# Kernel optimization log

Hardware: AMD Instinct MI355X
Metric: run time of the kernel (lower is better)

The kernel has to match this reference:

```python
import jax, jax.numpy as jnp
import numpy as np
import math

INPUT_DIM = 1024
QUERY_DIM = 1024
VALUE_DIM = 1024

def setup_inputs() -> dict:
    key = jax.random.key(0)
    ks = jax.random.split(key, 7)
    N, T, D = 4, 4096, INPUT_DIM
    s_in = 1.0 / math.sqrt(D)
    X = jax.random.normal(ks[0], (N, T, D), dtype=jnp.float32)
    # torch.nn.Linear weights: (out, in), init ~ U(-1/sqrt(in), 1/sqrt(in))
    Wq = jax.random.uniform(ks[1], (QUERY_DIM, D), jnp.float32, -s_in, s_in)
    bq = jax.random.uniform(ks[2], (QUERY_DIM,), jnp.float32, -s_in, s_in)
    Wk = jax.random.uniform(ks[3], (QUERY_DIM, D), jnp.float32, -s_in, s_in)
    bk = jax.random.uniform(ks[4], (QUERY_DIM,), jnp.float32, -s_in, s_in)
    Wv = jax.random.uniform(ks[5], (VALUE_DIM, D), jnp.float32, -s_in, s_in)
    bv = jax.random.uniform(ks[6], (VALUE_DIM,), jnp.float32, -s_in, s_in)
    return {"X": X, "Wq": Wq, "bq": bq, "Wk": Wk, "bk": bk, "Wv": Wv, "bv": bv}

def reference(X, Wq, bq, Wk, bk, Wv, bv):
    N, T, D = X.shape
    q = jnp.einsum('ntd,qd->ntq', X, Wq) + bq  # (N,T,Q)
    k = jnp.einsum('ntd,qd->ntq', X, Wk) + bk  # (N,T,Q)
    v = jnp.einsum('ntd,vd->ntv', X, Wv) + bv  # (N,T,V)
    # NOTE: original scales by sqrt(D) = sqrt(input_dim), not sqrt(query_dim)
    scores = jnp.einsum('ntq,nsq->nts', q, k) / jnp.sqrt(jnp.asarray(D, X.dtype))
    attn = jax.nn.softmax(scores, axis=-1)  # (N,T,T)
    return jnp.einsum('nts,nsv->ntv', attn, v)
```

## Files before the change

### kernel.cpp

```cpp
#include <hip/hip_runtime.h>
#include <stdint.h>

typedef unsigned short u16;
typedef unsigned char u8;
typedef unsigned int u32;
typedef short shortx8 __attribute__((ext_vector_type(8)));
typedef float floatx4 __attribute__((ext_vector_type(4)));
typedef int intx4 __attribute__((ext_vector_type(4)));
typedef int intx8 __attribute__((ext_vector_type(8)));

__device__ __forceinline__ u16 f2bf(float f) {
    u32 u = __builtin_bit_cast(u32, f);
    u = (u + 0x7fffu + ((u >> 16) & 1u)) >> 16;
    return (u16)u;
}

#if defined(__has_builtin)
#  if __has_builtin(__builtin_amdgcn_cvt_pk_fp8_f32)
#    define HAVE_CVT_FP8 1
#  endif
#  if __has_builtin(__builtin_amdgcn_global_load_lds)
#    define HAVE_GLL 1
#  endif
#endif
#ifndef HAVE_CVT_FP8
#  define HAVE_CVT_FP8 0
#endif
#ifndef HAVE_GLL
#  define HAVE_GLL 0
#endif

__device__ __forceinline__ u8 f2fp8(float f) {
#if HAVE_CVT_FP8
    return (u8)(__builtin_amdgcn_cvt_pk_fp8_f32(f, f, 0, false) & 0xff);
#else
    u32 u = __builtin_bit_cast(u32, f);
    u32 s = (u >> 24) & 0x80u;
    u32 m = u & 0x7fffffffu;
    if (m >= 0x43e00000u) return (u8)(s | 0x7eu);
    if (m < 0x3c800000u) {
        int q = __float2int_rn(__builtin_bit_cast(float, m) * 512.f);
        return (u8)(s | (u32)q);
    }
    u32 r = m + 0x7ffffu + ((m >> 20) & 1u);
    u32 code = (((r >> 23) - 120u) << 3) | ((r >> 20) & 7u);
    if (code > 0x7eu) code = 0x7eu;
    return (u8)(s | code);
#endif
}

#if HAVE_GLL
__device__ __forceinline__ void gload_lds16(const void* g, void* l) {
    __builtin_amdgcn_global_load_lds(
        (const __attribute__((address_space(1))) u32*)g,
        (__attribute__((address_space(3))) u32*)l,
        16, 0, 0);
}
#endif

template <typename OutT, int MODE, int SWZ>
__global__ __launch_bounds__(256, 2) void gemm_bt(
    const u16* __restrict__ Ag, const u16* __restrict__ Bg, OutT* __restrict__ Cg,
    int lda, int ldb, int ldc, int K,
    const float* __restrict__ aux, float scale,
    long long sAz, long long sBz, long long sCz, long long sXz,
    int swz_nhalf)
{
    __shared__ u16 smem[4][128 * 32];

    int z, mb, nb;
    if constexpr (SWZ) {
        const int f = blockIdx.x, xcd = f & 7, g = f >> 3;
        z = xcd >> 1;
        mb = g & 31;
        nb = (xcd & 1) * swz_nhalf + (g >> 5);
    } else {
        z = blockIdx.z; mb = blockIdx.y; nb = blockIdx.x;
    }
    const int m0 = mb * 128, n0 = nb * 128;

    const u16* A = Ag + (long long)z * sAz;
    const u16* B = Bg + (long long)z * sBz;
    OutT* C = Cg + (long long)z * sCz;
    const float* auxp = aux ? aux + (long long)z * sXz : nullptr;

    const int tid = threadIdx.x, lane = tid & 63, wv = tid >> 6;

    const int srow = lane >> 2;
    const int schunk = (lane & 3) * 8;
    const u16* gA0 = A + (size_t)(m0 + wv * 16 + srow) * lda + schunk;
    const u16* gA1 = gA0 + (size_t)64 * lda;
    const u16* gB0 = B + (size_t)(n0 + wv * 16 + srow) * ldb + schunk;
    const u16* gB1 = gB0 + (size_t)64 * ldb;
    const int wb = wv * 512;

    const int wm = (wv & 1) * 64, wn = (wv >> 1) * 64;
    const int mi = lane & 15, kq = lane >> 4;

    floatx4 acc[4][4] = {};

    for (int k0 = 0; k0 < K; k0 += 64) {
#if HAVE_GLL
        gload_lds16(gA0,      &smem[0][wb]);
        gload_lds16(gA1,      &smem[0][2048 + wb]);
        gload_lds16(gA0 + 32, &smem[1][wb]);
        gload_lds16(gA1 + 32, &smem[1][2048 + wb]);
        gload_lds16(gB0,      &smem[2][wb]);
        gload_lds16(gB1,      &smem[2][2048 + wb]);
        gload_lds16(gB0 + 32, &smem[3][wb]);
        gload_lds16(gB1 + 32, &smem[3][2048 + wb]);
#else
        *(shortx8*)(&smem[0][wb] + lane * 8)        = *(const shortx8*)gA0;
        *(shortx8*)(&smem[0][2048 + wb] + lane * 8) = *(const shortx8*)gA1;
        *(shortx8*)(&smem[1][wb] + lane * 8)        = *(const shortx8*)(gA0 + 32);
        *(shortx8*)(&smem[1][2048 + wb] + lane * 8) = *(const shortx8*)(gA1 + 32);
        *(shortx8*)(&smem[2][wb] + lane * 8)        = *(const shortx8*)gB0;
        *(shortx8*)(&smem[2][2048 + wb] + lane * 8) = *(const shortx8*)gB1;
        *(shortx8*)(&smem[3][wb] + lane * 8)        = *(const shortx8*)(gB0 + 32);
        *(shortx8*)(&smem[3][2048 + wb] + lane * 8) = *(const shortx8*)(gB1 + 32);
#endif
        gA0 += 64; gA1 += 64; gB0 += 64; gB1 += 64;
        __syncthreads();

#pragma unroll
        for (int h = 0; h < 2; h++) {
            const u16* Ap = smem[h];
            const u16* Bp = smem[2 + h];
            shortx8 af[4], bfr[4];
#pragma unroll
            for (int i = 0; i < 4; i++)
                af[i] = *(const shortx8*)(Ap + (wm + i * 16 + mi) * 32 + kq * 8);
#pragma unroll
            for (int j = 0; j < 4; j++)
                bfr[j] = *(const shortx8*)(Bp + (wn + j * 16 + mi) * 32 + kq * 8);
#pragma unroll
            for (int i = 0; i < 4; i++)
#pragma unroll
                for (int j = 0; j < 4; j++)
                    acc[i][j] = __builtin_amdgcn_mfma_f32_16x16x32_bf16(
                        af[i], bfr[j], acc[i][j], 0, 0, 0);
        }
        __syncthreads();
    }

    float cb[4];
    if constexpr (MODE == 1) {
#pragma unroll
        for (int j = 0; j < 4; j++) cb[j] = auxp[n0 + wn + j * 16 + mi];
    }

    if constexpr (sizeof(OutT) == 2) {
        u16* ct = &smem[0][0];
#pragma unroll
        for (int i = 0; i < 4; i++) {
#pragma unroll
            for (int r = 0; r < 4; r++) {
                const int lrow = wm + i * 16 + kq * 4 + r;
                float radd = 0.f;
                if constexpr (MODE == 2) radd = auxp[m0 + lrow];
#pragma unroll
                for (int j = 0; j < 4; j++) {
                    float v = acc[i][j][r];
                    if constexpr (MODE == 1) v += cb[j];
                    if constexpr (MODE == 2) v += radd;
                    ct[lrow * 128 + wn + j * 16 + mi] = f2bf(v);
                }
            }
        }
        __syncthreads();
#pragma unroll
        for (int it = 0; it < 8; it++) {
            const int fl = (it * 256 + tid) * 8;
            const int row = fl >> 7, col = fl & 127;
            *(uint4*)(C + (size_t)(m0 + row) * ldc + n0 + col) =
                *(const uint4*)(ct + fl);
        }
    } else if constexpr (sizeof(OutT) == 1) {
        u8* ct = (u8*)&smem[0][0];
#pragma unroll
        for (int i = 0; i < 4; i++) {
#pragma unroll
            for (int r = 0; r < 4; r++) {
                const int lrow = wm + i * 16 + kq * 4 + r;
#pragma unroll
                for (int j = 0; j < 4; j++) {
                    float v = acc[i][j][r];
                    if constexpr (MODE == 1) v += cb[j];
                    ct[lrow * 128 + wn + j * 16 + mi] = f2fp8(v);
                }
            }
        }
        __syncthreads();
        u8* base = (u8*)Cg + ((size_t)mb * 16 + nb) * 16384;
#pragma unroll
        for (int it = 0; it < 4; it++) {
            const int fl = (it * 256 + tid) * 16;
            const int row = fl >> 7, c = (fl >> 4) & 7;
            *(uint4*)(base + row * 128 + ((c ^ (row & 7)) << 4)) =
                *(const uint4*)(ct + fl);
        }
    } else {
#pragma unroll
        for (int i = 0; i < 4; i++) {
#pragma unroll
            for (int r = 0; r < 4; r++) {
                const int row = m0 + wm + i * 16 + kq * 4 + r;
                float rmul = 1.f;
                if constexpr (MODE == 4) rmul = 1.0f / auxp[row];
                OutT* crow = C + (size_t)row * ldc;
#pragma unroll
                for (int j = 0; j < 4; j++) {
                    const int col = n0 + wn + j * 16 + mi;
                    crow[col] = acc[i][j][r] * rmul;
                }
            }
        }
    }
}

__global__ __launch_bounds__(512, 2) void gemm_pv256(
    const u16* __restrict__ Pg, const u16* __restrict__ Vt,
    float* __restrict__ outg, const float* __restrict__ sums, int T, int NT)
{
    __shared__ u8 smem[2][65536];

    const int f = blockIdx.x, xcd = f & 7, g = f >> 3;
    const int z = xcd >> 1;
    const int nb = (xcd & 1) * 2 + (g >> 4);
    const int mb = g & 15;
    const int m0 = mb * 256, n0 = nb * 256;

    const u8* Pz = (const u8*)(Pg + (size_t)z * T * T);
    const u8* Vz = (const u8*)(Vt + (size_t)z * T);
    const float* sumz = sums + (size_t)z * T;

    const int tid = threadIdx.x, lane = tid & 63, wv = tid >> 6;
    const int wr = wv >> 2, wc = wv & 3;
    const int mi = lane & 15, kq = lane >> 4;

    const int srow = lane >> 3;
    const int schunk = ((lane & 7) ^ srow) << 4;
    const size_t ldPb = (size_t)T * 2, ldVb = (size_t)NT * 2;
    const u8* gsrc;
    size_t grstride;
    int lds_r0;
    if (wv < 4) {
        gsrc = Pz + (size_t)(m0 + wv * 64 + srow) * ldPb + schunk;
        grstride = ldPb * 8;
        lds_r0 = wv * 8192;
    } else {
        gsrc = Vz + (size_t)(n0 + (wv - 4) * 64 + srow) * ldVb + schunk;
        grstride = ldVb * 8;
        lds_r0 = 32768 + (wv - 4) * 8192;
    }

    const int csw0 = ((0 * 4 + kq) ^ (mi & 7)) << 4;
    const int csw1 = ((1 * 4 + kq) ^ (mi & 7)) << 4;

    floatx4 acc[8][4] = {};

    auto stage = [&](int slot, int kt) {
        const u8* s0 = gsrc + (size_t)kt * 128;
        u8* l0 = &smem[slot][lds_r0];
#if HAVE_GLL
#pragma unroll
        for (int q = 0; q < 8; q++)
            gload_lds16(s0 + (size_t)q * grstride, l0 + q * 1024);
#else
#pragma unroll
        for (int q = 0; q < 8; q++)
            *(uint4*)(l0 + q * 1024 + lane * 16) =
                *(const uint4*)(s0 + (size_t)q * grstride);
#endif
    };

    stage(0, 0);
    __syncthreads();

    for (int kt = 0; kt < 64; kt++) {
        const int s = kt & 1;
        if (kt < 63) stage(s ^ 1, kt + 1);
        __builtin_amdgcn_sched_barrier(0);

        const u8* Ab = &smem[s][0];
        const u8* Bb = &smem[s][32768];

        shortx8 bfr[4][2];
#pragma unroll
        for (int nj = 0; nj < 4; nj++) {
            const u8* p = Bb + (wc * 64 + nj * 16 + mi) * 128;
            bfr[nj][0] = *(const shortx8*)(p + csw0);
            bfr[nj][1] = *(const shortx8*)(p + csw1);
        }
#pragma unroll
        for (int mh = 0; mh < 2; mh++) {
            shortx8 af[4][2];
#pragma unroll
            for (int fi = 0; fi < 4; fi++) {
                const u8* p = Ab + (wr * 128 + (mh * 4 + fi) * 16 + mi) * 128;
                af[fi][0] = *(const shortx8*)(p + csw0);
                af[fi][1] = *(const shortx8*)(p + csw1);
            }
            __builtin_amdgcn_s_setprio(1);
#pragma unroll
            for (int ks = 0; ks < 2; ks++)
#pragma unroll
                for (int fi = 0; fi < 4; fi++)
#pragma unroll
                    for (int nj = 0; nj < 4; nj++)
                        acc[mh * 4 + fi][nj] = __builtin_amdgcn_mfma_f32_16x16x32_bf16(
                            af[fi][ks], bfr[nj][ks], acc[mh * 4 + fi][nj], 0, 0, 0);
            __builtin_amdgcn_s_setprio(0);
        }
        __syncthreads();
    }

#pragma unroll
    for (int fr = 0; fr < 8; fr++) {
#pragma unroll
        for (int r = 0; r < 4; r++) {
            const int row = m0 + wr * 128 + fr * 16 + kq * 4 + r;
            const float rmul = 1.0f / sumz[row];
            float* crow = outg + ((size_t)z * T + row) * 1024 + n0 + wc * 64 + mi;
#pragma unroll
            for (int nj = 0; nj < 4; nj++)
                crow[nj * 16] = acc[fr][nj][r] * rmul;
        }
    }
}

__device__ __forceinline__ intx8 cat8(intx4 a, intx4 b) {
    return __builtin_shufflevector(a, b, 0, 1, 2, 3, 4, 5, 6, 7);
}

template <int SWZ>
__global__ __launch_bounds__(256, 1) void gemm_fp8_scores(
    const u8* __restrict__ QKt, u16* __restrict__ Pg,
    float* __restrict__ sums, float scale, int T)
{
    __shared__ u8 smem[4][16384];

    int z, mb, nb;
    if constexpr (SWZ) {
        const int f = blockIdx.x, xcd = f & 7, g = f >> 3;
        z = xcd >> 1;
        const int s = g >> 7, t = g & 127;
        mb = (s << 3) | (t & 7);
        nb = (xcd & 1) * 16 + (t >> 3);
    } else {
        z = blockIdx.z; mb = blockIdx.y; nb = blockIdx.x;
    }
    const int m0 = mb * 128, n0 = nb * 128;

    const u8* At = QKt + ((size_t)(z * 32 + mb) * 16) * 16384;
    const u8* Bt = QKt + ((size_t)(z * 32 + nb) * 16 + 8) * 16384;
    u16* P = Pg + (size_t)z * T * T;
    float* sumz = sums + (size_t)z * T;

    const int tid = threadIdx.x, lane = tid & 63, wv = tid >> 6;
    const int wm = (wv & 1) * 64, wn = (wv >> 1) * 64;
    const int mi = lane & 15, kq = lane >> 4;
    const int xm = mi & 7;
    const int off0 = ((2 * kq) ^ xm) * 16;
    const int off1 = ((2 * kq + 1) ^ xm) * 16;

    const u8* gA = At + wv * 4096 + lane * 16;
    const u8* gB = Bt + wv * 4096 + lane * 16;

    floatx4 acc[4][4] = {};

#if HAVE_GLL
#pragma unroll
    for (int i = 0; i < 4; i++) {
        gload_lds16(gA + i * 1024, &smem[0][wv * 4096] + i * 1024);
        gload_lds16(gB + i * 1024, &smem[1][wv * 4096] + i * 1024);
    }
#else
#pragma unroll
    for (int i = 0; i < 4; i++) {
        *(uint4*)(&smem[0][wv * 4096] + i * 1024 + lane * 16) = *(const uint4*)(gA + i * 1024);
        *(uint4*)(&smem[1][wv * 4096] + i * 1024 + lane * 16) = *(const uint4*)(gB + i * 1024);
    }
#endif
    gA += 16384; gB += 16384;
    __syncthreads();

    int cur = 0;
    for (int kp = 0; kp < 8; kp++) {
        const int nxt = cur ^ 2;
        if (kp < 7) {
#if HAVE_GLL
#pragma unroll
            for (int i = 0; i < 4; i++) {
                gload_lds16(gA + i * 1024, &smem[nxt][wv * 4096] + i * 1024);
                gload_lds16(gB + i * 1024, &smem[nxt + 1][wv * 4096] + i * 1024);
            }
#else
#pragma unroll
            for (int i = 0; i < 4; i++) {
                *(uint4*)(&smem[nxt][wv * 4096] + i * 1024 + lane * 16) = *(const uint4*)(gA + i * 1024);
                *(uint4*)(&smem[nxt + 1][wv * 4096] + i * 1024 + lane * 16) = *(const uint4*)(gB + i * 1024);
            }
#endif
            gA += 16384; gB += 16384;
        }
        __builtin_amdgcn_sched_barrier(0);

        const u8* Bp = &smem[cur + 1][0];
        intx8 af[4];
#pragma unroll
        for (int i = 0; i < 4; i++) {
            const u8* p = &smem[cur][(wm + i * 16 + mi) * 128];
            af[i] = cat8(*(const intx4*)(p + off0), *(const intx4*)(p + off1));
        }
#pragma unroll
        for (int j = 0; j < 4; j++) {
            const u8* p = Bp + (wn + j * 16 + mi) * 128;
            const intx8 bfr = cat8(*(const intx4*)(p + off0), *(const intx4*)(p + off1));
#pragma unroll
            for (int i = 0; i < 4; i++)
                acc[i][j] = __builtin_amdgcn_mfma_scale_f32_16x16x128_f8f6f4(
                    af[i], bfr, acc[i][j], 0, 0,
                    0, 0x7f7f7f7f, 0, 0x7f7f7f7f);
        }
        __syncthreads();
        cur = nxt;
    }

    u16* ct = (u16*)&smem[0][0];
#pragma unroll
    for (int i = 0; i < 4; i++) {
#pragma unroll
        for (int r = 0; r < 4; r++) {
            const int lrow = wm + i * 16 + kq * 4 + r;
            float rs = 0.f;
#pragma unroll
            for (int j = 0; j < 4; j++) {
                float v = __expf(acc[i][j][r] * scale);
                rs += v;
                ct[lrow * 128 + wn + j * 16 + mi] = f2bf(v);
            }
            rs += __shfl_xor(rs, 1);
            rs += __shfl_xor(rs, 2);
            rs += __shfl_xor(rs, 4);
            rs += __shfl_xor(rs, 8);
            if (mi == 0) atomicAdd(&sumz[m0 + lrow], rs);
        }
    }
    __syncthreads();
#pragma unroll
    for (int it = 0; it < 8; it++) {
        const int fl = (it * 256 + tid) * 8;
        const int row = fl >> 7, col = fl & 127;
        *(uint4*)(P + (size_t)(m0 + row) * T + n0 + col) = *(const uint4*)(ct + fl);
    }
}

__global__ __launch_bounds__(256) void cvt_bf16(const float* __restrict__ s,
                                                u16* __restrict__ d, int n8)
{
    int i = blockIdx.x * 256 + threadIdx.x;
    if (i >= n8) return;
    const float4* sp = (const float4*)s;
    float4 a = sp[2 * i], b = sp[2 * i + 1];
    uint4 o;
    o.x = (u32)f2bf(a.x) | ((u32)f2bf(a.y) << 16);
    o.y = (u32)f2bf(a.z) | ((u32)f2bf(a.w) << 16);
    o.z = (u32)f2bf(b.x) | ((u32)f2bf(b.y) << 16);
    o.w = (u32)f2bf(b.z) | ((u32)f2bf(b.w) << 16);
    *(uint4*)(d + 8 * i) = o;
}

__global__ void concat2(const float* __restrict__ a, const float* __restrict__ b,
                        float* __restrict__ d, int n)
{
    int i = blockIdx.x * 256 + threadIdx.x;
    if (i < n) d[i] = a[i];
    else if (i < 2 * n) d[i] = b[i - n];
}

extern "C" void kernel_launch(void* const* d_in, const int* in_sizes, int n_in,
                              void* d_out, int out_size, void* d_ws, size_t ws_size,
                              hipStream_t stream)
{
    const float* X  = (const float*)d_in[0];
    const float* Wq = (const float*)d_in[1];
    const float* bq = (const float*)d_in[2];
    const float* Wk = (const float*)d_in[3];
    const float* bk = (const float*)d_in[4];
    const float* Wv = (const float*)d_in[5];
    const float* bv = (const float*)d_in[6];
    float* out = (float*)d_out;

    const int T = 4096, NT = 4 * T;
    const long long TL = T;

    char* ws = (char*)d_ws;
    size_t off = 0;
    auto alloc = [&](size_t bytes) {
        char* p = ws + off;
        off += (bytes + 255) & ~(size_t)255;
        return p;
    };
    u16*   Wqk  = (u16*)alloc((size_t)2048 * 1024 * 2);
    u16*   Wvb  = (u16*)alloc((size_t)1024 * 1024 * 2);
    float* bqk  = (float*)alloc(2048 * 4);
    u8*    QKt  = (u8*)alloc((size_t)128 * 16 * 16384);
    u16*   Vt   = (u16*)alloc((size_t)1024 * NT * 2);
    float* sums = (float*)alloc((size_t)NT * 4);
    size_t pbase = off;
    u16*   Xb   = (u16*)alloc((size_t)NT * 1024 * 2);
    u16*   P    = Xb;

    const size_t need_batched = pbase + (size_t)4 * T * T * 2;
    const bool batched = ws_size >= need_batched;

    cvt_bf16<<<dim3((NT * 1024 / 8 + 255) / 256), dim3(256), 0, stream>>>(X, Xb, NT * 1024 / 8);
    cvt_bf16<<<dim3(512), dim3(256), 0, stream>>>(Wq, Wqk, 1024 * 1024 / 8);
    cvt_bf16<<<dim3(512), dim3(256), 0, stream>>>(Wk, Wqk + 1024 * 1024, 1024 * 1024 / 8);
    cvt_bf16<<<dim3(512), dim3(256), 0, stream>>>(Wv, Wvb, 1024 * 1024 / 8);
    concat2<<<dim3(8), dim3(256), 0, stream>>>(bq, bk, bqk, 1024);
    hipMemsetAsync(sums, 0, (size_t)NT * 4, stream);

    gemm_bt<u8, 1, 0><<<dim3(16, 128, 1), dim3(256), 0, stream>>>(
        Xb, Wqk, QKt, 1024, 1024, 0, 1024, bqk, 0.f, 0, 0, 0, 0, 0);

    gemm_bt<u16, 2, 0><<<dim3(128, 8, 1), dim3(256), 0, stream>>>(
        Wvb, Xb, Vt, 1024, 1024, NT, 1024, bv, 0.f, 0, 0, 0, 0, 0);

    if (batched) {
        gemm_fp8_scores<1><<<dim3(4096), dim3(256), 0, stream>>>(
            QKt, P, sums, 0.03125f, T);
        gemm_pv256<<<dim3(256), dim3(512), 0, stream>>>(
            P, Vt, out, sums, T, NT);
    } else {
        for (int z = 0; z < 4; z++) {
            gemm_fp8_scores<0><<<dim3(32, 32, 1), dim3(256), 0, stream>>>(
                QKt + (size_t)z * 32 * 16 * 16384, P, sums + (size_t)z * T, 0.03125f, T);
            gemm_bt<float, 4, 0><<<dim3(8, 32, 1), dim3(256), 0, stream>>>(
                P, Vt + (size_t)z * T, out + (size_t)z * T * 1024,
                T, NT, 1024, T, sums + (size_t)z * T, 0.f, 0, 0, 0, 0, 0);
        }
    }
    (void)in_sizes; (void)n_in; (void)out_size;
}
```

Baseline: 509.5 us.

## Deepen fp8 scores GEMM to a four-stage LDS ring with explicit vmcnt waits

Replaces the double-buffered LDS pipeline in the fp8 scores kernel with a four-slot ring buffer that keeps three K-stages in flight. It uses explicit s_waitcnt vmcnt thresholds and a single barrier per iteration, so each tile's global loads have more time to land before use. The intent is to hide global-to-LDS latency over the short eight-step K loop. In exchange, LDS use doubles to 128KB per block, and correctness now depends on hand-tuned vmcnt counts that only hold on the global_load_lds path.

```diff
diff --git a/kernel.cpp b/kernel.cpp
--- a/kernel.cpp
+++ b/kernel.cpp
@@ -338,7 +338,7 @@
     const u8* __restrict__ QKt, u16* __restrict__ Pg,
     float* __restrict__ sums, float scale, int T)
 {
-    __shared__ u8 smem[4][16384];
+    __shared__ u8 smem[4][32768];
 
     int z, mb, nb;
     if constexpr (SWZ) {
@@ -369,48 +369,48 @@
 
     floatx4 acc[4][4] = {};
 
+    auto stageP = [&](int b) {
 #if HAVE_GLL
 #pragma unroll
-    for (int i = 0; i < 4; i++) {
-        gload_lds16(gA + i * 1024, &smem[0][wv * 4096] + i * 1024);
-        gload_lds16(gB + i * 1024, &smem[1][wv * 4096] + i * 1024);
-    }
+        for (int i = 0; i < 4; i++) {
+            gload_lds16(gA + i * 1024, &smem[b][wv * 4096] + i * 1024);
+            gload_lds16(gB + i * 1024, &smem[b][16384 + wv * 4096] + i * 1024);
+        }
 #else
 #pragma unroll
-    for (int i = 0; i < 4; i++) {
-        *(uint4*)(&smem[0][wv * 4096] + i * 1024 + lane * 16) = *(const uint4*)(gA + i * 1024);
-        *(uint4*)(&smem[1][wv * 4096] + i * 1024 + lane * 16) = *(const uint4*)(gB + i * 1024);
-    }
-#endif
-    gA += 16384; gB += 16384;
-    __syncthreads();
-
-    int cur = 0;
+        for (int i = 0; i < 4; i++) {
+            *(uint4*)(&smem[b][wv * 4096] + i * 1024 + lane * 16) =
+                *(const uint4*)(gA + i * 1024);
+            *(uint4*)(&smem[b][16384 + wv * 4096] + i * 1024 + lane * 16) =
+                *(const uint4*)(gB + i * 1024);
+        }
+#endif
+        gA += 16384; gB += 16384;
+    };
+
+    stageP(0);
+    stageP(1);
+    stageP(2);
+
+#pragma unroll
     for (int kp = 0; kp < 8; kp++) {
-        const int nxt = cur ^ 2;
-        if (kp < 7) {
 #if HAVE_GLL
-#pragma unroll
-            for (int i = 0; i < 4; i++) {
-                gload_lds16(gA + i * 1024, &smem[nxt][wv * 4096] + i * 1024);
-                gload_lds16(gB + i * 1024, &smem[nxt + 1][wv * 4096] + i * 1024);
-            }
+        if (kp <= 5)      asm volatile("s_waitcnt vmcnt(16)" ::: "memory");
+        else if (kp == 6) asm volatile("s_waitcnt vmcnt(8)" ::: "memory");
+        else              asm volatile("s_waitcnt vmcnt(0)" ::: "memory");
+        __builtin_amdgcn_s_barrier();
 #else
-#pragma unroll
-            for (int i = 0; i < 4; i++) {
-                *(uint4*)(&smem[nxt][wv * 4096] + i * 1024 + lane * 16) = *(const uint4*)(gA + i * 1024);
-                *(uint4*)(&smem[nxt + 1][wv * 4096] + i * 1024 + lane * 16) = *(const uint4*)(gB + i * 1024);
-            }
-#endif
-            gA += 16384; gB += 16384;
-        }
+        __syncthreads();
+#endif
+        if (kp < 5) stageP((kp + 3) & 3);
         __builtin_amdgcn_sched_barrier(0);
 
-        const u8* Bp = &smem[cur + 1][0];
+        const u8* Ap = &smem[kp & 3][0];
+        const u8* Bp = &smem[kp & 3][16384];
         intx8 af[4];
 #pragma unroll
         for (int i = 0; i < 4; i++) {
-            const u8* p = &smem[cur][(wm + i * 16 + mi) * 128];
+            const u8* p = Ap + (wm + i * 16 + mi) * 128;
             af[i] = cat8(*(const intx4*)(p + off0), *(const intx4*)(p + off1));
         }
 #pragma unroll
@@ -423,8 +423,6 @@
                     af[i], bfr, acc[i][j], 0, 0,
                     0, 0x7f7f7f7f, 0, 0x7f7f7f7f);
         }
-        __syncthreads();
-        cur = nxt;
     }
 
     u16* ct = (u16*)&smem[0][0];
```

Result: faster. 495.1 us (-2.8%).
